# Kernel tuning notes

Hardware: AMD Instinct MI355X
Metric: run time of the kernel (lower is better)

## Reference

```python
import jax, jax.numpy as jnp
import numpy as np

Q_HEADS, KV_HEADS, D_K, D_V = 16, 4, 128, 128
GROUPS = Q_HEADS // KV_HEADS


def setup_inputs() -> dict:
    key = jax.random.key(0)
    ks = jax.random.split(key, 7)
    b, s, d = 2, 2048, 2048
    scale = 1.0 / np.sqrt(d).astype(np.float32)
    return {
        "Q": jax.random.normal(ks[0], (b, s, d), jnp.float32),
        "K": jax.random.normal(ks[1], (b, s, d), jnp.float32),
        "V": jax.random.normal(ks[2], (b, s, d), jnp.float32),
        "Wq": jax.random.normal(ks[3], (d, D_K * Q_HEADS), jnp.float32) * scale,
        "Wk": jax.random.normal(ks[4], (d, D_K * KV_HEADS), jnp.float32) * scale,
        "Wv": jax.random.normal(ks[5], (d, D_V * KV_HEADS), jnp.float32) * scale,
        "Wo": jax.random.normal(ks[6], (D_V * KV_HEADS, d), jnp.float32) * scale,
    }


def reference(Q, K, V, Wq, Wk, Wv, Wo):
    b, lq, _ = Q.shape
    lk = K.shape[1]
    # projections -> (b, heads, len, d)
    q = (Q @ Wq).reshape(b, lq, Q_HEADS, D_K).transpose(0, 2, 1, 3)
    k = (K @ Wk).reshape(b, lk, KV_HEADS, D_K).transpose(0, 2, 1, 3)
    v = (V @ Wv).reshape(b, lk, KV_HEADS, D_V).transpose(0, 2, 1, 3)
    # GQA quirk: scores summed over group dim g before softmax
    qr = q.reshape(b, GROUPS, KV_HEADS, lq, D_K)
    scores = jnp.einsum('bghqd,bhkd->bhqk', qr, k) / jnp.asarray(D_K ** 0.5, q.dtype)
    causal = jnp.tril(jnp.ones((lq, lk), bool))
    scores = jnp.where(causal[None, None], scores, jnp.asarray(-1e9, scores.dtype))
    attn = jax.nn.softmax(scores, axis=-1)  # (b, kv_heads, lq, lk)
    out = jnp.einsum('bhqk,bhkd->bhqd', attn, v)  # (b, kv_heads, lq, d_v)
    out = out.transpose(0, 2, 1, 3).reshape(b, lq, KV_HEADS * D_V)
    return out @ Wo
```

## Files before the change

### kernel.cpp

```cpp
#include <hip/hip_runtime.h>
#include <hip/hip_bf16.h>

typedef __attribute__((ext_vector_type(8))) short short8;
typedef __attribute__((ext_vector_type(4))) float f32x4;

#define MFMA16 __builtin_amdgcn_mfma_f32_16x16x32_bf16

__device__ inline unsigned short f2bf(float f) {
  __hip_bfloat16 h = __float2bfloat16(f);
  unsigned short u;
  __builtin_memcpy(&u, &h, 2);
  return u;
}

__device__ inline float bf2f(unsigned short u) {
  unsigned int x = ((unsigned int)u) << 16;
  float f;
  __builtin_memcpy(&f, &x, 4);
  return f;
}

__device__ inline void storeC(unsigned short* p, float v) { *p = f2bf(v); }
__device__ inline void storeC(float* p, float v) { *p = v; }

__device__ inline void gload16(const void* g, void* l) {
  __builtin_amdgcn_global_load_lds(
      (const __attribute__((address_space(1))) unsigned int*)g,
      (__attribute__((address_space(3))) unsigned int*)l,
      16, 0, 0);
}

__global__ __launch_bounds__(256)
void wqsum_t(const float* __restrict__ wq, unsigned short* __restrict__ dst) {
  __shared__ float t[64][65];
  const int n0 = blockIdx.x * 64, d0 = blockIdx.y * 64;
  const int tid = threadIdx.x;
#pragma unroll
  for (int it = 0; it < 16; ++it) {
    const int idx = it * 256 + tid;
    const int dd = idx >> 6, nn = idx & 63;
    const float* p = wq + (size_t)(d0 + dd) * 2048 + n0 + nn;
    t[dd][nn] = p[0] + p[512] + p[1024] + p[1536];
  }
  __syncthreads();
#pragma unroll
  for (int it = 0; it < 16; ++it) {
    const int idx = it * 256 + tid;
    const int nn = idx >> 6, dd = idx & 63;
    dst[(size_t)(n0 + nn) * 2048 + d0 + dd] = f2bf(t[dd][nn]);
  }
}

__global__ __launch_bounds__(256)
void transpose_w(const float* __restrict__ src, unsigned short* __restrict__ dst,
                 int R, int C) {
  __shared__ float t[64][65];
  const int c0 = blockIdx.x * 64, r0 = blockIdx.y * 64;
  const int tid = threadIdx.x;
#pragma unroll
  for (int it = 0; it < 16; ++it) {
    const int idx = it * 256 + tid;
    const int r = idx >> 6, c = idx & 63;
    t[r][c] = src[(size_t)(r0 + r) * C + c0 + c];
  }
  __syncthreads();
#pragma unroll
  for (int it = 0; it < 16; ++it) {
    const int idx = it * 256 + tid;
    const int rr = idx >> 6, cc = idx & 63;
    dst[(size_t)(c0 + rr) * R + r0 + cc] = f2bf(t[cc][rr]);
  }
}

__global__ __launch_bounds__(256)
void vtrans(const unsigned short* __restrict__ pC, unsigned short* __restrict__ vt) {
  __shared__ unsigned short t[64][72];
  const int s0 = blockIdx.x * 64;
  const int d0 = blockIdx.y * 64;
  const int bh = blockIdx.z;
  const int brow = (bh >> 2) * 2048;
  const int h = bh & 3;
  const int tid = threadIdx.x;
  const unsigned short* va = pC + 4194304;
  const unsigned short* vb = pC + 6291456 + 4194304;
#pragma unroll
  for (int it = 0; it < 2; ++it) {
    const int idx = it * 256 + tid;
    const int s = idx >> 3;
    const int dd = (idx & 7) << 3;
    const size_t off = (size_t)(brow + s0 + s) * 512 + h * 128 + d0 + dd;
    const short8 xa = *(const short8*)(va + off);
    const short8 xb = *(const short8*)(vb + off);
    short8 o;
#pragma unroll
    for (int e = 0; e < 8; ++e)
      o[e] = (short)f2bf(bf2f((unsigned short)xa[e]) + bf2f((unsigned short)xb[e]));
    *(short8*)&t[s][dd] = o;
  }
  __syncthreads();
#pragma unroll
  for (int it = 0; it < 2; ++it) {
    const int idx = it * 256 + tid;
    const int dd = idx >> 3;
    const int ss = (idx & 7) << 3;
    short8 o;
#pragma unroll
    for (int e = 0; e < 8; ++e) o[e] = (short)t[ss + e][dd];
    *(short8*)(vt + ((size_t)bh * 128 + d0 + dd) * 2048 + s0 + ss) = o;
  }
}

template <bool AF32, typename CT, int KS>
__global__ __launch_bounds__(256)
void gemm_bt(const void* A0, const void* A1, const void* A2,
             const unsigned short* __restrict__ Bt, CT* __restrict__ C,
             int K, int N, size_t sB, size_t sC) {
  __shared__ unsigned short As[AF32 ? 1 : 2][128 * 64];
  __shared__ unsigned short Bs[2][128 * 64];

  const int tid = threadIdx.x;
  const int lane = tid & 63;
  const int wv = tid >> 6;
  const int wm = (wv >> 1) << 6;
  const int wn = (wv & 1) << 6;
  const int l15 = lane & 15;
  const int l4 = lane >> 4;
  const int lsw = (l15 & 7) << 4;

  const int nwg = gridDim.x;
  const int bid = blockIdx.x;
  const int job = (bid & 7) * (nwg >> 3) + (bid >> 3);
  const int ntile = N >> 7;
  const int per_ks = nwg / KS;
  const int ks = (KS > 1) ? (job / per_ks) : 0;
  const int jj = job - ks * per_ks;
  const int z = jj / (32 * ntile);
  const int rem = jj - z * 32 * ntile;
  const int m0 = (rem / ntile) << 7;
  const int n0 = (rem % ntile) << 7;
  const int kbeg = ks * (K / KS);
  const int kend = kbeg + K / KS;

  const void* Az = (z == 0) ? A0 : (z == 1) ? A1 : A2;
  const unsigned short* Ab = (const unsigned short*)Az;
  const float* Af = (const float*)Az;
  const unsigned short* Bz = Bt + sB * (size_t)z;

  const f32x4 zero = {0.f, 0.f, 0.f, 0.f};
  f32x4 acc[4][4];
#pragma unroll
  for (int i = 0; i < 4; ++i)
#pragma unroll
    for (int j = 0; j < 4; ++j) acc[i][j] = zero;

  const int srow = tid >> 3;
  const int scol = (tid & 7) << 3;
  const int scolsw = scol ^ ((srow & 7) << 3);

  float4 ar[8];

  auto issueB = [&](int buf, int k0) {
#pragma unroll
    for (int s = 0; s < 4; ++s) {
      const unsigned short* bsrc =
          Bz + (size_t)(n0 + srow + s * 32) * K + k0 + scolsw;
      gload16(bsrc, (char*)&Bs[buf][0] + tid * 16 + s * 4096);
    }
  };
  auto issueA16 = [&](int buf, int k0) {
#pragma unroll
    for (int s = 0; s < 4; ++s) {
      const unsigned short* asrc =
          Ab + (size_t)(m0 + srow + s * 32) * K + k0 + scolsw;
      gload16(asrc, (char*)&As[buf][0] + tid * 16 + s * 4096);
    }
  };
  auto loadA = [&](int k0) {
#pragma unroll
    for (int s = 0; s < 4; ++s) {
      const float* asrc = Af + (size_t)(m0 + srow + s * 32) * K + k0 + scol;
      ar[2 * s] = *(const float4*)(asrc);
      ar[2 * s + 1] = *(const float4*)(asrc + 4);
    }
  };
  auto writeA = [&]() {
#pragma unroll
    for (int s = 0; s < 4; ++s) {
      short8 o;
      o[0] = (short)f2bf(ar[2 * s].x); o[1] = (short)f2bf(ar[2 * s].y);
      o[2] = (short)f2bf(ar[2 * s].z); o[3] = (short)f2bf(ar[2 * s].w);
      o[4] = (short)f2bf(ar[2 * s + 1].x); o[5] = (short)f2bf(ar[2 * s + 1].y);
      o[6] = (short)f2bf(ar[2 * s + 1].z); o[7] = (short)f2bf(ar[2 * s + 1].w);
      *(short8*)((char*)&As[0][0] + (srow + s * 32) * 128 + scolsw * 2) = o;
    }
  };

  if constexpr (AF32) loadA(kbeg); else issueA16(0, kbeg);
  issueB(0, kbeg);

  int cur = 0;
  for (int k0 = kbeg; k0 < kend; k0 += 64) {
    const bool more = (k0 + 64 < kend);
    asm volatile("s_waitcnt vmcnt(0)" ::: "memory");
    if constexpr (AF32) {
      writeA();
      if (more) { issueB(cur ^ 1, k0 + 64); loadA(k0 + 64); }
      asm volatile("s_waitcnt lgkmcnt(0)" ::: "memory");
    } else {
      if (more) { issueA16(cur ^ 1, k0 + 64); issueB(cur ^ 1, k0 + 64); }
    }
    __builtin_amdgcn_s_barrier();
    const unsigned short* as = AF32 ? &As[0][0] : &As[cur][0];
#pragma unroll
    for (int kk = 0; kk < 2; ++kk) {
      const int kb = (kk * 64 + (l4 << 4)) ^ lsw;
      short8 a[4], b[4];
#pragma unroll
      for (int i = 0; i < 4; ++i)
        a[i] = *(const short8*)((const char*)as + (wm + i * 16 + l15) * 128 + kb);
#pragma unroll
      for (int j = 0; j < 4; ++j)
        b[j] = *(const short8*)((const char*)&Bs[cur][0] +
                                (wn + j * 16 + l15) * 128 + kb);
#pragma unroll
      for (int i = 0; i < 4; ++i)
#pragma unroll
        for (int j = 0; j < 4; ++j)
          acc[i][j] = MFMA16(a[i], b[j], acc[i][j], 0, 0, 0);
    }
    __builtin_amdgcn_s_barrier();
    cur ^= 1;
  }

  CT* Cz = C + sC * (size_t)(ks * 3 + z);
#pragma unroll
  for (int i = 0; i < 4; ++i) {
    const int row0 = m0 + wm + i * 16 + (l4 << 2);
#pragma unroll
    for (int j = 0; j < 4; ++j) {
      const int col = n0 + wn + j * 16 + l15;
#pragma unroll
      for (int r = 0; r < 4; ++r)
        storeC(&Cz[(size_t)(row0 + r) * N + col], acc[i][j][r]);
    }
  }
}

__global__ __launch_bounds__(256)
void qkv_combine(const unsigned short* __restrict__ pC,
                 unsigned short* __restrict__ dst) {
  const size_t COUNT = 4194304;
  const size_t OFF = 6291456;
  size_t i = ((size_t)blockIdx.x * 256 + threadIdx.x) * 8;
  const size_t stride = (size_t)gridDim.x * 256 * 8;
  for (; i < COUNT; i += stride) {
    const short8 a = *(const short8*)(pC + i);
    const short8 b = *(const short8*)(pC + OFF + i);
    short8 o;
#pragma unroll
    for (int e = 0; e < 8; ++e)
      o[e] = (short)f2bf(bf2f((unsigned short)a[e]) + bf2f((unsigned short)b[e]));
    *(short8*)(dst + i) = o;
  }
}

__global__ __launch_bounds__(128, 1)
void attn_split(const unsigned short* __restrict__ qh,
                const unsigned short* __restrict__ kh,
                const unsigned short* __restrict__ vt,
                unsigned short* __restrict__ Oh,
                unsigned short* __restrict__ pO,
                float* __restrict__ pml) {
  __shared__ unsigned short P_lds[2][32][36];
  const int tid = threadIdx.x;
  const int lane = tid & 63;
  const int wave = tid >> 6;
  const int l15 = lane & 15;
  const int l4 = lane >> 4;
  const int bh = blockIdx.x & 7;
  const int jid = 143 - (int)(blockIdx.x >> 3);
  const int brow = (bh >> 2) * 2048;
  const int h = bh & 3;

  int j = jid, g = 0;
  while (j >= 2 * (g + 1) * (g + 2)) ++g;
  const int rem = j - 2 * g * (g + 1);
  const int r_ = rem / (g + 1);
  const int c_ = rem - r_ * (g + 1);
  const int qt = 4 * g + r_;
  const int k_begin = c_ << 8;
  const int k_end = (c_ == g) ? (qt + 1) * 64 : ((c_ + 1) << 8);
  const int qrow_w = qt * 64 + wave * 32;
  const float SCALE2 = 0.127517424f;

  short8 qf[2][4];
#pragma unroll
  for (int m = 0; m < 2; ++m) {
    const unsigned short* qp =
        qh + (size_t)(brow + qrow_w + m * 16 + l15) * 512 + h * 128 + (l4 << 3);
#pragma unroll
    for (int kk = 0; kk < 4; ++kk) qf[m][kk] = *(const short8*)(qp + kk * 32);
  }

  short8 oneb;
#pragma unroll
  for (int e = 0; e < 8; ++e) oneb[e] = (short)0x3F80;

  const f32x4 zero = {0.f, 0.f, 0.f, 0.f};
  f32x4 o_acc[2][8];
  f32x4 l_acc[2];
#pragma unroll
  for (int m = 0; m < 2; ++m) {
    l_acc[m] = zero;
#pragma unroll
    for (int i = 0; i < 8; ++i) o_acc[m][i] = zero;
  }

  const int nt = (k_end - k_begin) >> 5;
  for (int t = 0; t < nt; ++t) {
    const int kbase = k_begin + t * 32;
    if (kbase > qrow_w + 31) continue;
    short8 vb[8];
#pragma unroll
    for (int d8 = 0; d8 < 8; ++d8)
      vb[d8] = *(const short8*)(
          vt + ((size_t)bh * 128 + d8 * 16 + l15) * 2048 + kbase + (l4 << 3));
    short8 kf[2][4];
#pragma unroll
    for (int n = 0; n < 2; ++n) {
      const unsigned short* kp =
          kh + (size_t)(brow + kbase + n * 16 + l15) * 512 + h * 128 + (l4 << 3);
#pragma unroll
      for (int kk = 0; kk < 4; ++kk) kf[n][kk] = *(const short8*)(kp + kk * 32);
    }
    f32x4 sa[2][2];
    sa[0][0] = zero; sa[0][1] = zero; sa[1][0] = zero; sa[1][1] = zero;
#pragma unroll
    for (int n = 0; n < 2; ++n)
#pragma unroll
      for (int kk = 0; kk < 4; ++kk) {
        sa[0][n] = MFMA16(qf[0][kk], kf[n][kk], sa[0][n], 0, 0, 0);
        sa[1][n] = MFMA16(qf[1][kk], kf[n][kk], sa[1][n], 0, 0, 0);
      }
    const bool need_mask = (kbase + 31 > qrow_w);
    float p[2][2][4];
#pragma unroll
    for (int m = 0; m < 2; ++m)
#pragma unroll
      for (int n = 0; n < 2; ++n)
#pragma unroll
        for (int r = 0; r < 4; ++r) {
          const float v = exp2f(sa[m][n][r] * SCALE2 - 24.f);
          bool msk = false;
          if (need_mask) {
            const int kc = kbase + n * 16 + l15;
            const int qr = qrow_w + m * 16 + (l4 << 2) + r;
            msk = (kc > qr);
          }
          p[m][n][r] = msk ? 0.f : v;
        }
#pragma unroll
    for (int m = 0; m < 2; ++m)
#pragma unroll
      for (int n = 0; n < 2; ++n)
#pragma unroll
        for (int r = 0; r < 4; ++r)
          P_lds[wave][m * 16 + (l4 << 2) + r][n * 16 + l15] = f2bf(p[m][n][r]);
    short8 pa[2];
#pragma unroll
    for (int m = 0; m < 2; ++m)
      pa[m] = *(const short8*)((const char*)&P_lds[wave][0][0] +
                               (m * 16 + l15) * 72 + (l4 << 4));
    l_acc[0] = MFMA16(pa[0], oneb, l_acc[0], 0, 0, 0);
    l_acc[1] = MFMA16(pa[1], oneb, l_acc[1], 0, 0, 0);
#pragma unroll
    for (int d8 = 0; d8 < 8; ++d8) {
      o_acc[0][d8] = MFMA16(pa[0], vb[d8], o_acc[0][d8], 0, 0, 0);
      o_acc[1][d8] = MFMA16(pa[1], vb[d8], o_acc[1][d8], 0, 0, 0);
    }
  }

  if (g == 0) {
#pragma unroll
    for (int m = 0; m < 2; ++m)
#pragma unroll
      for (int d8 = 0; d8 < 8; ++d8)
#pragma unroll
        for (int r = 0; r < 4; ++r) {
          const int row = brow + qrow_w + m * 16 + (l4 << 2) + r;
          Oh[(size_t)row * 512 + h * 128 + d8 * 16 + l15] =
              f2bf(o_acc[m][d8][r] / l_acc[m][r]);
        }
  } else {
    const int slot = bh * 144 + jid;
    unsigned short* po = pO + (size_t)slot * 64 * 128;
#pragma unroll
    for (int m = 0; m < 2; ++m)
#pragma unroll
      for (int d8 = 0; d8 < 8; ++d8)
#pragma unroll
        for (int r = 0; r < 4; ++r) {
          const int row = wave * 32 + m * 16 + (l4 << 2) + r;
          po[row * 128 + d8 * 16 + l15] = f2bf(o_acc[m][d8][r]);
        }
    if (l15 == 0) {
#pragma unroll
      for (int m = 0; m < 2; ++m)
#pragma unroll
        for (int r = 0; r < 4; ++r) {
          const int row = wave * 32 + m * 16 + (l4 << 2) + r;
          pml[((size_t)slot * 64 + row) * 2 + 0] = 0.f;
          pml[((size_t)slot * 64 + row) * 2 + 1] = l_acc[m][r];
        }
    }
  }
}

__global__ __launch_bounds__(256)
void attn_combine(const unsigned short* __restrict__ pO,
                  const float* __restrict__ pml,
                  unsigned short* __restrict__ Oh) {
  const int bh = blockIdx.y;
  const int qt = 4 + blockIdx.x;
  const int g = qt >> 2;
  const int nch = g + 1;
  const int base = 2 * g * (g + 1) + (qt & 3) * (g + 1);
  const int slot0 = bh * 144 + base;
  const int brow = (bh >> 2) * 2048;
  const int h = bh & 3;
#pragma unroll
  for (int u = 0; u < 4; ++u) {
    const int unit = u * 256 + threadIdx.x;
    const int row = unit >> 4;
    const int c8 = (unit & 15) << 3;
    float M = -1e30f;
    for (int c = 0; c < nch; ++c)
      M = fmaxf(M, pml[((size_t)(slot0 + c) * 64 + row) * 2]);
    float L = 0.f;
    float acc[8] = {0.f, 0.f, 0.f, 0.f, 0.f, 0.f, 0.f, 0.f};
    for (int c = 0; c < nch; ++c) {
      const float mc = pml[((size_t)(slot0 + c) * 64 + row) * 2];
      const float lc = pml[((size_t)(slot0 + c) * 64 + row) * 2 + 1];
      const float w = exp2f(mc - M);
      L += w * lc;
      const short8 ov =
          *(const short8*)(pO + ((size_t)(slot0 + c) * 64 + row) * 128 + c8);
#pragma unroll
      for (int e = 0; e < 8; ++e) acc[e] += w * bf2f((unsigned short)ov[e]);
    }
    const float inv = 1.f / L;
    short8 o;
#pragma unroll
    for (int e = 0; e < 8; ++e) o[e] = (short)f2bf(acc[e] * inv);
    *(short8*)(Oh + (size_t)(brow + qt * 64 + row) * 512 + h * 128 + c8) = o;
  }
}

extern "C" void kernel_launch(void* const* d_in, const int* in_sizes, int n_in,
                              void* d_out, int out_size, void* d_ws, size_t ws_size,
                              hipStream_t stream) {
  const float* Q  = (const float*)d_in[0];
  const float* K_ = (const float*)d_in[1];
  const float* V  = (const float*)d_in[2];
  const float* Wq = (const float*)d_in[3];
  const float* Wk = (const float*)d_in[4];
  const float* Wv = (const float*)d_in[5];
  const float* Wo = (const float*)d_in[6];
  float* out = (float*)d_out;

  char* ws = (char*)d_ws;
  unsigned short* Wt  = (unsigned short*)ws;
  unsigned short* WoT = (unsigned short*)(ws + 6291456);
  unsigned short* qh  = (unsigned short*)(ws + 8388608);
  unsigned short* kh  = qh + 2097152;
  unsigned short* Oh  = qh + 3 * 2097152;
  unsigned short* vt  = (unsigned short*)(ws + 25165824);
  unsigned short* pO  = (unsigned short*)(ws + 29360128);
  float*          pml = (float*)(ws + 48234496);
  unsigned short* pC  = (unsigned short*)(ws + 20971520);

  wqsum_t<<<dim3(8, 32), 256, 0, stream>>>(Wq, Wt);
  transpose_w<<<dim3(8, 32), 256, 0, stream>>>(Wk, Wt + 1048576, 2048, 512);
  transpose_w<<<dim3(8, 32), 256, 0, stream>>>(Wv, Wt + 2097152, 2048, 512);
  transpose_w<<<dim3(32, 8), 256, 0, stream>>>(Wo, WoT, 512, 2048);

  gemm_bt<true, unsigned short, 2><<<768, 256, 0, stream>>>(
      Q, K_, V, Wt, pC, 2048, 512, 1048576, 2097152);
  qkv_combine<<<1024, 256, 0, stream>>>(pC, qh);
  vtrans<<<dim3(32, 2, 8), 256, 0, stream>>>(pC, vt);

  attn_split<<<1152, 128, 0, stream>>>(qh, kh, vt, Oh, pO, pml);
  attn_combine<<<dim3(28, 8), 256, 0, stream>>>(pO, pml, Oh);

  gemm_bt<false, float, 1><<<512, 256, 0, stream>>>(
      Oh, Oh, Oh, WoT, out, 512, 2048, 0, 0);
}
```

Baseline: 146.7 us.

## Double-buffer fp32 A tiles in LDS and prefetch two tiles ahead

In the fp32-input GEMM path, the A tile now gets two LDS buffers and two register staging sets, so global loads of A run two k-tiles ahead. The bf16 conversion and LDS write for the next tile happen after the MFMA work on the current tile. Partial vmcnt waits replace full drains. This is meant to hide global load latency that the single-buffer scheme left exposed, at the cost of more LDS and registers, which can lower occupancy.

```diff
diff --git a/kernel.cpp b/kernel.cpp
--- a/kernel.cpp
+++ b/kernel.cpp
@@ -115,7 +115,7 @@
 void gemm_bt(const void* A0, const void* A1, const void* A2,
              const unsigned short* __restrict__ Bt, CT* __restrict__ C,
              int K, int N, size_t sB, size_t sC) {
-  __shared__ unsigned short As[AF32 ? 1 : 2][128 * 64];
+  __shared__ unsigned short As[2][128 * 64];
   __shared__ unsigned short Bs[2][128 * 64];
 
   const int tid = threadIdx.x;
@@ -157,8 +157,6 @@
   const int scol = (tid & 7) << 3;
   const int scolsw = scol ^ ((srow & 7) << 3);
 
-  float4 ar[8];
-
   auto issueB = [&](int buf, int k0) {
 #pragma unroll
     for (int s = 0; s < 4; ++s) {
@@ -175,7 +173,7 @@
       gload16(asrc, (char*)&As[buf][0] + tid * 16 + s * 4096);
     }
   };
-  auto loadA = [&](int k0) {
+  auto loadAr = [&](float4 (&ar)[8], int k0) {
 #pragma unroll
     for (int s = 0; s < 4; ++s) {
       const float* asrc = Af + (size_t)(m0 + srow + s * 32) * K + k0 + scol;
@@ -183,7 +181,7 @@
       ar[2 * s + 1] = *(const float4*)(asrc + 4);
     }
   };
-  auto writeA = [&]() {
+  auto writeAr = [&](int buf, float4 (&ar)[8]) {
 #pragma unroll
     for (int s = 0; s < 4; ++s) {
       short8 o;
@@ -191,33 +189,18 @@
       o[2] = (short)f2bf(ar[2 * s].z); o[3] = (short)f2bf(ar[2 * s].w);
       o[4] = (short)f2bf(ar[2 * s + 1].x); o[5] = (short)f2bf(ar[2 * s + 1].y);
       o[6] = (short)f2bf(ar[2 * s + 1].z); o[7] = (short)f2bf(ar[2 * s + 1].w);
-      *(short8*)((char*)&As[0][0] + (srow + s * 32) * 128 + scolsw * 2) = o;
+      *(short8*)((char*)&As[buf][0] + (srow + s * 32) * 128 + scolsw * 2) = o;
     }
   };
-
-  if constexpr (AF32) loadA(kbeg); else issueA16(0, kbeg);
-  issueB(0, kbeg);
-
-  int cur = 0;
-  for (int k0 = kbeg; k0 < kend; k0 += 64) {
-    const bool more = (k0 + 64 < kend);
-    asm volatile("s_waitcnt vmcnt(0)" ::: "memory");
-    if constexpr (AF32) {
-      writeA();
-      if (more) { issueB(cur ^ 1, k0 + 64); loadA(k0 + 64); }
-      asm volatile("s_waitcnt lgkmcnt(0)" ::: "memory");
-    } else {
-      if (more) { issueA16(cur ^ 1, k0 + 64); issueB(cur ^ 1, k0 + 64); }
-    }
-    __builtin_amdgcn_s_barrier();
-    const unsigned short* as = AF32 ? &As[0][0] : &As[cur][0];
+  auto mfma_tile = [&](int cur) {
 #pragma unroll
     for (int kk = 0; kk < 2; ++kk) {
       const int kb = (kk * 64 + (l4 << 4)) ^ lsw;
       short8 a[4], b[4];
 #pragma unroll
       for (int i = 0; i < 4; ++i)
-        a[i] = *(const short8*)((const char*)as + (wm + i * 16 + l15) * 128 + kb);
+        a[i] = *(const short8*)((const char*)&As[cur][0] +
+                                (wm + i * 16 + l15) * 128 + kb);
 #pragma unroll
       for (int j = 0; j < 4; ++j)
         b[j] = *(const short8*)((const char*)&Bs[cur][0] +
@@ -228,8 +211,55 @@
         for (int j = 0; j < 4; ++j)
           acc[i][j] = MFMA16(a[i], b[j], acc[i][j], 0, 0, 0);
     }
-    __builtin_amdgcn_s_barrier();
-    cur ^= 1;
+  };
+
+  const int ntiles = (kend - kbeg) >> 6;
+
+  if constexpr (AF32) {
+    float4 arA[8], arB[8];
+    loadAr(arA, kbeg);
+    issueB(0, kbeg);
+    if (ntiles > 1) {
+      loadAr(arB, kbeg + 64);
+      asm volatile("s_waitcnt vmcnt(8)" ::: "memory");
+    } else {
+      asm volatile("s_waitcnt vmcnt(0)" ::: "memory");
+    }
+    writeAr(0, arA);
+
+    auto step = [&](int i, int cur, float4 (&arW)[8], float4 (&arL)[8]) {
+      if (i >= ntiles) return;
+      const bool haveB = (i + 1 < ntiles);
+      const bool haveA = (i + 2 < ntiles);
+      if (haveB) issueB(cur ^ 1, kbeg + (i + 1) * 64);
+      if (haveA) loadAr(arL, kbeg + (i + 2) * 64);
+      asm volatile("s_waitcnt lgkmcnt(0)" ::: "memory");
+      __builtin_amdgcn_s_barrier();
+      mfma_tile(cur);
+      if (haveB) {
+        if (haveA) asm volatile("s_waitcnt vmcnt(8)" ::: "memory");
+        else       asm volatile("s_waitcnt vmcnt(0)" ::: "memory");
+        __builtin_amdgcn_s_barrier();
+        writeAr(cur ^ 1, arW);
+      }
+    };
+    for (int i = 0; i < ntiles; i += 2) {
+      step(i, 0, arB, arA);
+      step(i + 1, 1, arA, arB);
+    }
+  } else {
+    issueA16(0, kbeg);
+    issueB(0, kbeg);
+    int cur = 0;
+    for (int k0 = kbeg; k0 < kend; k0 += 64) {
+      const bool more = (k0 + 64 < kend);
+      asm volatile("s_waitcnt vmcnt(0)" ::: "memory");
+      if (more) { issueA16(cur ^ 1, k0 + 64); issueB(cur ^ 1, k0 + 64); }
+      __builtin_amdgcn_s_barrier();
+      mfma_tile(cur);
+      __builtin_amdgcn_s_barrier();
+      cur ^= 1;
+    }
   }
 
   CT* Cz = C + sC * (size_t)(ks * 3 + z);
```

Measured after the change: 154.8 us. 1.06x slower.

## Use 3-way split-K for QKV GEMM and 4-wave 16-row attention blocks

Applied to the files above, without the earlier changes.

The QKV projection GEMM moves from a 2-way to a 3-way K split, launching more workgroups, and a third partial slot is summed in qkv_combine and vtrans. The f32-A path drops B double-buffering to cut LDS use. The attention split kernel now uses 4 waves of 16 query rows each instead of 2 waves of 32, which lowers per-wave register pressure so launch bounds can allow multiple blocks per CU. The workspace layout is reshuffled so the larger partial buffer overlaps regions that are already consumed. The costs are extra partial-sum traffic and less pipelining in the GEMM's B loads.

```diff
diff --git a/kernel.cpp b/kernel.cpp
--- a/kernel.cpp
+++ b/kernel.cpp
@@ -81,20 +81,24 @@
   const int brow = (bh >> 2) * 2048;
   const int h = bh & 3;
   const int tid = threadIdx.x;
-  const unsigned short* va = pC + 4194304;
-  const unsigned short* vb = pC + 6291456 + 4194304;
+  const unsigned short* v0 = pC + 4194304;
+  const unsigned short* v1 = pC + 6291456 + 4194304;
+  const unsigned short* v2 = pC + 12582912 + 4194304;
 #pragma unroll
   for (int it = 0; it < 2; ++it) {
     const int idx = it * 256 + tid;
     const int s = idx >> 3;
     const int dd = (idx & 7) << 3;
     const size_t off = (size_t)(brow + s0 + s) * 512 + h * 128 + d0 + dd;
-    const short8 xa = *(const short8*)(va + off);
-    const short8 xb = *(const short8*)(vb + off);
+    const short8 xa = *(const short8*)(v0 + off);
+    const short8 xb = *(const short8*)(v1 + off);
+    const short8 xc = *(const short8*)(v2 + off);
     short8 o;
 #pragma unroll
     for (int e = 0; e < 8; ++e)
-      o[e] = (short)f2bf(bf2f((unsigned short)xa[e]) + bf2f((unsigned short)xb[e]));
+      o[e] = (short)f2bf(bf2f((unsigned short)xa[e]) +
+                         bf2f((unsigned short)xb[e]) +
+                         bf2f((unsigned short)xc[e]));
     *(short8*)&t[s][dd] = o;
   }
   __syncthreads();
@@ -116,7 +120,7 @@
              const unsigned short* __restrict__ Bt, CT* __restrict__ C,
              int K, int N, size_t sB, size_t sC) {
   __shared__ unsigned short As[AF32 ? 1 : 2][128 * 64];
-  __shared__ unsigned short Bs[2][128 * 64];
+  __shared__ unsigned short Bs[AF32 ? 1 : 2][128 * 64];
 
   const int tid = threadIdx.x;
   const int lane = tid & 63;
@@ -138,8 +142,10 @@
   const int rem = jj - z * 32 * ntile;
   const int m0 = (rem / ntile) << 7;
   const int n0 = (rem % ntile) << 7;
-  const int kbeg = ks * (K / KS);
-  const int kend = kbeg + K / KS;
+  const int steps = K >> 6;
+  const int per = (steps + KS - 1) / KS;
+  const int sb = ks * per, se = (ks + 1) * per < steps ? (ks + 1) * per : steps;
+  const int kbeg = sb << 6, kend = se << 6;
 
   const void* Az = (z == 0) ? A0 : (z == 1) ? A1 : A2;
   const unsigned short* Ab = (const unsigned short*)Az;
@@ -194,30 +200,15 @@
       *(short8*)((char*)&As[0][0] + (srow + s * 32) * 128 + scolsw * 2) = o;
     }
   };
-
-  if constexpr (AF32) loadA(kbeg); else issueA16(0, kbeg);
-  issueB(0, kbeg);
-
-  int cur = 0;
-  for (int k0 = kbeg; k0 < kend; k0 += 64) {
-    const bool more = (k0 + 64 < kend);
-    asm volatile("s_waitcnt vmcnt(0)" ::: "memory");
-    if constexpr (AF32) {
-      writeA();
-      if (more) { issueB(cur ^ 1, k0 + 64); loadA(k0 + 64); }
-      asm volatile("s_waitcnt lgkmcnt(0)" ::: "memory");
-    } else {
-      if (more) { issueA16(cur ^ 1, k0 + 64); issueB(cur ^ 1, k0 + 64); }
-    }
-    __builtin_amdgcn_s_barrier();
-    const unsigned short* as = AF32 ? &As[0][0] : &As[cur][0];
+  auto mfma_tile = [&](int cur) {
 #pragma unroll
     for (int kk = 0; kk < 2; ++kk) {
       const int kb = (kk * 64 + (l4 << 4)) ^ lsw;
       short8 a[4], b[4];
 #pragma unroll
       for (int i = 0; i < 4; ++i)
-        a[i] = *(const short8*)((const char*)as + (wm + i * 16 + l15) * 128 + kb);
+        a[i] = *(const short8*)((const char*)&As[cur][0] +
+                                (wm + i * 16 + l15) * 128 + kb);
 #pragma unroll
       for (int j = 0; j < 4; ++j)
         b[j] = *(const short8*)((const char*)&Bs[cur][0] +
@@ -228,8 +219,31 @@
         for (int j = 0; j < 4; ++j)
           acc[i][j] = MFMA16(a[i], b[j], acc[i][j], 0, 0, 0);
     }
-    __builtin_amdgcn_s_barrier();
-    cur ^= 1;
+  };
+
+  if constexpr (AF32) {
+    loadA(kbeg);
+    for (int k0 = kbeg; k0 < kend; k0 += 64) {
+      writeA();
+      issueB(0, k0);
+      if (k0 + 64 < kend) loadA(k0 + 64);
+      __syncthreads();
+      mfma_tile(0);
+      __syncthreads();
+    }
+  } else {
+    issueA16(0, kbeg);
+    issueB(0, kbeg);
+    int cur = 0;
+    for (int k0 = kbeg; k0 < kend; k0 += 64) {
+      const bool more = (k0 + 64 < kend);
+      asm volatile("s_waitcnt vmcnt(0)" ::: "memory");
+      if (more) { issueA16(cur ^ 1, k0 + 64); issueB(cur ^ 1, k0 + 64); }
+      __builtin_amdgcn_s_barrier();
+      mfma_tile(cur);
+      __builtin_amdgcn_s_barrier();
+      cur ^= 1;
+    }
   }
 
   CT* Cz = C + sC * (size_t)(ks * 3 + z);
@@ -250,28 +264,31 @@
 void qkv_combine(const unsigned short* __restrict__ pC,
                  unsigned short* __restrict__ dst) {
   const size_t COUNT = 4194304;
-  const size_t OFF = 6291456;
+  const size_t SLOT = 6291456;
   size_t i = ((size_t)blockIdx.x * 256 + threadIdx.x) * 8;
   const size_t stride = (size_t)gridDim.x * 256 * 8;
   for (; i < COUNT; i += stride) {
     const short8 a = *(const short8*)(pC + i);
-    const short8 b = *(const short8*)(pC + OFF + i);
+    const short8 b = *(const short8*)(pC + SLOT + i);
+    const short8 c = *(const short8*)(pC + 2 * SLOT + i);
     short8 o;
 #pragma unroll
     for (int e = 0; e < 8; ++e)
-      o[e] = (short)f2bf(bf2f((unsigned short)a[e]) + bf2f((unsigned short)b[e]));
+      o[e] = (short)f2bf(bf2f((unsigned short)a[e]) +
+                         bf2f((unsigned short)b[e]) +
+                         bf2f((unsigned short)c[e]));
     *(short8*)(dst + i) = o;
   }
 }
 
-__global__ __launch_bounds__(128, 1)
+__global__ __launch_bounds__(256, 3)
 void attn_split(const unsigned short* __restrict__ qh,
                 const unsigned short* __restrict__ kh,
                 const unsigned short* __restrict__ vt,
                 unsigned short* __restrict__ Oh,
                 unsigned short* __restrict__ pO,
                 float* __restrict__ pml) {
-  __shared__ unsigned short P_lds[2][32][36];
+  __shared__ unsigned short P_lds[4][16][36];
   const int tid = threadIdx.x;
   const int lane = tid & 63;
   const int wave = tid >> 6;
@@ -290,16 +307,15 @@
   const int qt = 4 * g + r_;
   const int k_begin = c_ << 8;
   const int k_end = (c_ == g) ? (qt + 1) * 64 : ((c_ + 1) << 8);
-  const int qrow_w = qt * 64 + wave * 32;
+  const int qrow_w = qt * 64 + wave * 16;
   const float SCALE2 = 0.127517424f;
 
-  short8 qf[2][4];
-#pragma unroll
-  for (int m = 0; m < 2; ++m) {
+  short8 qf[4];
+  {
     const unsigned short* qp =
-        qh + (size_t)(brow + qrow_w + m * 16 + l15) * 512 + h * 128 + (l4 << 3);
-#pragma unroll
-    for (int kk = 0; kk < 4; ++kk) qf[m][kk] = *(const short8*)(qp + kk * 32);
+        qh + (size_t)(brow + qrow_w + l15) * 512 + h * 128 + (l4 << 3);
+#pragma unroll
+    for (int kk = 0; kk < 4; ++kk) qf[kk] = *(const short8*)(qp + kk * 32);
   }
 
   short8 oneb;
@@ -307,111 +323,95 @@
   for (int e = 0; e < 8; ++e) oneb[e] = (short)0x3F80;
 
   const f32x4 zero = {0.f, 0.f, 0.f, 0.f};
-  f32x4 o_acc[2][8];
-  f32x4 l_acc[2];
-#pragma unroll
-  for (int m = 0; m < 2; ++m) {
-    l_acc[m] = zero;
-#pragma unroll
-    for (int i = 0; i < 8; ++i) o_acc[m][i] = zero;
-  }
+  f32x4 o_acc[8];
+  f32x4 l_acc = zero;
+#pragma unroll
+  for (int i = 0; i < 8; ++i) o_acc[i] = zero;
 
   const int nt = (k_end - k_begin) >> 5;
   for (int t = 0; t < nt; ++t) {
     const int kbase = k_begin + t * 32;
-    if (kbase > qrow_w + 31) continue;
-    short8 vb[8];
-#pragma unroll
-    for (int d8 = 0; d8 < 8; ++d8)
-      vb[d8] = *(const short8*)(
+    if (kbase > qrow_w + 15) continue;
+    short8 vb0[4];
+#pragma unroll
+    for (int d8 = 0; d8 < 4; ++d8)
+      vb0[d8] = *(const short8*)(
           vt + ((size_t)bh * 128 + d8 * 16 + l15) * 2048 + kbase + (l4 << 3));
-    short8 kf[2][4];
+    f32x4 sa[2];
+    sa[0] = zero; sa[1] = zero;
 #pragma unroll
     for (int n = 0; n < 2; ++n) {
+      short8 kf[4];
       const unsigned short* kp =
           kh + (size_t)(brow + kbase + n * 16 + l15) * 512 + h * 128 + (l4 << 3);
 #pragma unroll
-      for (int kk = 0; kk < 4; ++kk) kf[n][kk] = *(const short8*)(kp + kk * 32);
-    }
-    f32x4 sa[2][2];
-    sa[0][0] = zero; sa[0][1] = zero; sa[1][0] = zero; sa[1][1] = zero;
+      for (int kk = 0; kk < 4; ++kk) kf[kk] = *(const short8*)(kp + kk * 32);
+#pragma unroll
+      for (int kk = 0; kk < 4; ++kk)
+        sa[n] = MFMA16(qf[kk], kf[kk], sa[n], 0, 0, 0);
+    }
+    const bool need_mask = (kbase + 31 > qrow_w);
+    float p[2][4];
 #pragma unroll
     for (int n = 0; n < 2; ++n)
 #pragma unroll
-      for (int kk = 0; kk < 4; ++kk) {
-        sa[0][n] = MFMA16(qf[0][kk], kf[n][kk], sa[0][n], 0, 0, 0);
-        sa[1][n] = MFMA16(qf[1][kk], kf[n][kk], sa[1][n], 0, 0, 0);
+      for (int r = 0; r < 4; ++r) {
+        const float v = exp2f(sa[n][r] * SCALE2 - 24.f);
+        bool msk = false;
+        if (need_mask) {
+          const int kc = kbase + n * 16 + l15;
+          const int qr = qrow_w + (l4 << 2) + r;
+          msk = (kc > qr);
+        }
+        p[n][r] = msk ? 0.f : v;
       }
-    const bool need_mask = (kbase + 31 > qrow_w);
-    float p[2][2][4];
-#pragma unroll
-    for (int m = 0; m < 2; ++m)
-#pragma unroll
-      for (int n = 0; n < 2; ++n)
-#pragma unroll
-        for (int r = 0; r < 4; ++r) {
-          const float v = exp2f(sa[m][n][r] * SCALE2 - 24.f);
-          bool msk = false;
-          if (need_mask) {
-            const int kc = kbase + n * 16 + l15;
-            const int qr = qrow_w + m * 16 + (l4 << 2) + r;
-            msk = (kc > qr);
-          }
-          p[m][n][r] = msk ? 0.f : v;
-        }
-#pragma unroll
-    for (int m = 0; m < 2; ++m)
-#pragma unroll
-      for (int n = 0; n < 2; ++n)
-#pragma unroll
-        for (int r = 0; r < 4; ++r)
-          P_lds[wave][m * 16 + (l4 << 2) + r][n * 16 + l15] = f2bf(p[m][n][r]);
-    short8 pa[2];
-#pragma unroll
-    for (int m = 0; m < 2; ++m)
-      pa[m] = *(const short8*)((const char*)&P_lds[wave][0][0] +
-                               (m * 16 + l15) * 72 + (l4 << 4));
-    l_acc[0] = MFMA16(pa[0], oneb, l_acc[0], 0, 0, 0);
-    l_acc[1] = MFMA16(pa[1], oneb, l_acc[1], 0, 0, 0);
-#pragma unroll
-    for (int d8 = 0; d8 < 8; ++d8) {
-      o_acc[0][d8] = MFMA16(pa[0], vb[d8], o_acc[0][d8], 0, 0, 0);
-      o_acc[1][d8] = MFMA16(pa[1], vb[d8], o_acc[1][d8], 0, 0, 0);
-    }
+#pragma unroll
+    for (int n = 0; n < 2; ++n)
+#pragma unroll
+      for (int r = 0; r < 4; ++r)
+        P_lds[wave][(l4 << 2) + r][n * 16 + l15] = f2bf(p[n][r]);
+    short8 pa = *(const short8*)((const char*)&P_lds[wave][0][0] +
+                                 l15 * 72 + (l4 << 4));
+    short8 vb1[4];
+#pragma unroll
+    for (int d8 = 0; d8 < 4; ++d8)
+      vb1[d8] = *(const short8*)(
+          vt + ((size_t)bh * 128 + (d8 + 4) * 16 + l15) * 2048 + kbase + (l4 << 3));
+    l_acc = MFMA16(pa, oneb, l_acc, 0, 0, 0);
+#pragma unroll
+    for (int d8 = 0; d8 < 4; ++d8)
+      o_acc[d8] = MFMA16(pa, vb0[d8], o_acc[d8], 0, 0, 0);
+#pragma unroll
+    for (int d8 = 0; d8 < 4; ++d8)
+      o_acc[d8 + 4] = MFMA16(pa, vb1[d8], o_acc[d8 + 4], 0, 0, 0);
   }
 
   if (g == 0) {
 #pragma unroll
-    for (int m = 0; m < 2; ++m)
-#pragma unroll
-      for (int d8 = 0; d8 < 8; ++d8)
-#pragma unroll
-        for (int r = 0; r < 4; ++r) {
-          const int row = brow + qrow_w + m * 16 + (l4 << 2) + r;
-          Oh[(size_t)row * 512 + h * 128 + d8 * 16 + l15] =
-              f2bf(o_acc[m][d8][r] / l_acc[m][r]);
-        }
+    for (int d8 = 0; d8 < 8; ++d8)
+#pragma unroll
+      for (int r = 0; r < 4; ++r) {
+        const int row = brow + qrow_w + (l4 << 2) + r;
+        Oh[(size_t)row * 512 + h * 128 + d8 * 16 + l15] =
+            f2bf(o_acc[d8][r] / l_acc[r]);
+      }
   } else {
     const int slot = bh * 144 + jid;
     unsigned short* po = pO + (size_t)slot * 64 * 128;
 #pragma unroll
-    for (int m = 0; m < 2; ++m)
-#pragma unroll
-      for (int d8 = 0; d8 < 8; ++d8)
-#pragma unroll
-        for (int r = 0; r < 4; ++r) {
-          const int row = wave * 32 + m * 16 + (l4 << 2) + r;
-          po[row * 128 + d8 * 16 + l15] = f2bf(o_acc[m][d8][r]);
-        }
+    for (int d8 = 0; d8 < 8; ++d8)
+#pragma unroll
+      for (int r = 0; r < 4; ++r) {
+        const int row = wave * 16 + (l4 << 2) + r;
+        po[row * 128 + d8 * 16 + l15] = f2bf(o_acc[d8][r]);
+      }
     if (l15 == 0) {
 #pragma unroll
-      for (int m = 0; m < 2; ++m)
-#pragma unroll
-        for (int r = 0; r < 4; ++r) {
-          const int row = wave * 32 + m * 16 + (l4 << 2) + r;
-          pml[((size_t)slot * 64 + row) * 2 + 0] = 0.f;
-          pml[((size_t)slot * 64 + row) * 2 + 1] = l_acc[m][r];
-        }
+      for (int r = 0; r < 4; ++r) {
+        const int row = wave * 16 + (l4 << 2) + r;
+        pml[((size_t)slot * 64 + row) * 2 + 0] = 0.f;
+        pml[((size_t)slot * 64 + row) * 2 + 1] = l_acc[r];
+      }
     }
   }
 }
@@ -473,23 +473,23 @@
   unsigned short* WoT = (unsigned short*)(ws + 6291456);
   unsigned short* qh  = (unsigned short*)(ws + 8388608);
   unsigned short* kh  = qh + 2097152;
-  unsigned short* Oh  = qh + 3 * 2097152;
+  unsigned short* Oh  = (unsigned short*)(ws + 20971520);
   unsigned short* vt  = (unsigned short*)(ws + 25165824);
   unsigned short* pO  = (unsigned short*)(ws + 29360128);
   float*          pml = (float*)(ws + 48234496);
-  unsigned short* pC  = (unsigned short*)(ws + 20971520);
+  unsigned short* pC  = (unsigned short*)(ws + 8388608);
 
   wqsum_t<<<dim3(8, 32), 256, 0, stream>>>(Wq, Wt);
   transpose_w<<<dim3(8, 32), 256, 0, stream>>>(Wk, Wt + 1048576, 2048, 512);
   transpose_w<<<dim3(8, 32), 256, 0, stream>>>(Wv, Wt + 2097152, 2048, 512);
   transpose_w<<<dim3(32, 8), 256, 0, stream>>>(Wo, WoT, 512, 2048);
 
-  gemm_bt<true, unsigned short, 2><<<768, 256, 0, stream>>>(
+  gemm_bt<true, unsigned short, 3><<<1152, 256, 0, stream>>>(
       Q, K_, V, Wt, pC, 2048, 512, 1048576, 2097152);
   qkv_combine<<<1024, 256, 0, stream>>>(pC, qh);
   vtrans<<<dim3(32, 2, 8), 256, 0, stream>>>(pC, vt);
 
-  attn_split<<<1152, 128, 0, stream>>>(qh, kh, vt, Oh, pO, pml);
+  attn_split<<<1152, 256, 0, stream>>>(qh, kh, vt, Oh, pO, pml);
   attn_combine<<<dim3(28, 8), 256, 0, stream>>>(pO, pml, Oh);
 
   gemm_bt<false, float, 1><<<512, 256, 0, stream>>>(
```

Measured after the change: 190.1 us. +29.6%, slower.

## Pack Q/K/V into MFMA fragment order and double-buffer attention loads

Applied to the files above, without the earlier changes.

Replaces the row-major combine kernel and the V transpose with packing kernels that write Q, K and V directly in per-lane MFMA fragment order. Each lane's short8 is then contiguous, so attention loads are fully coalesced instead of strided row gathers. The attention inner loop also gains two-stage register double-buffering of K/V tiles, and fully masked tiles are dropped from the loop bound instead of being skipped with a branch. The cost is more registers under a 128-thread, 1-block launch bound, plus tighter workspace aliasing, since vpack reuses the partial-sum buffer.

```diff
diff --git a/kernel.cpp b/kernel.cpp
--- a/kernel.cpp
+++ b/kernel.cpp
@@ -69,44 +69,6 @@
     const int idx = it * 256 + tid;
     const int rr = idx >> 6, cc = idx & 63;
     dst[(size_t)(c0 + rr) * R + r0 + cc] = f2bf(t[cc][rr]);
-  }
-}
-
-__global__ __launch_bounds__(256)
-void vtrans(const unsigned short* __restrict__ pC, unsigned short* __restrict__ vt) {
-  __shared__ unsigned short t[64][72];
-  const int s0 = blockIdx.x * 64;
-  const int d0 = blockIdx.y * 64;
-  const int bh = blockIdx.z;
-  const int brow = (bh >> 2) * 2048;
-  const int h = bh & 3;
-  const int tid = threadIdx.x;
-  const unsigned short* va = pC + 4194304;
-  const unsigned short* vb = pC + 6291456 + 4194304;
-#pragma unroll
-  for (int it = 0; it < 2; ++it) {
-    const int idx = it * 256 + tid;
-    const int s = idx >> 3;
-    const int dd = (idx & 7) << 3;
-    const size_t off = (size_t)(brow + s0 + s) * 512 + h * 128 + d0 + dd;
-    const short8 xa = *(const short8*)(va + off);
-    const short8 xb = *(const short8*)(vb + off);
-    short8 o;
-#pragma unroll
-    for (int e = 0; e < 8; ++e)
-      o[e] = (short)f2bf(bf2f((unsigned short)xa[e]) + bf2f((unsigned short)xb[e]));
-    *(short8*)&t[s][dd] = o;
-  }
-  __syncthreads();
-#pragma unroll
-  for (int it = 0; it < 2; ++it) {
-    const int idx = it * 256 + tid;
-    const int dd = idx >> 3;
-    const int ss = (idx & 7) << 3;
-    short8 o;
-#pragma unroll
-    for (int e = 0; e < 8; ++e) o[e] = (short)t[ss + e][dd];
-    *(short8*)(vt + ((size_t)bh * 128 + d0 + dd) * 2048 + s0 + ss) = o;
   }
 }
 
@@ -247,27 +209,82 @@
 }
 
 __global__ __launch_bounds__(256)
-void qkv_combine(const unsigned short* __restrict__ pC,
-                 unsigned short* __restrict__ dst) {
-  const size_t COUNT = 4194304;
-  const size_t OFF = 6291456;
-  size_t i = ((size_t)blockIdx.x * 256 + threadIdx.x) * 8;
-  const size_t stride = (size_t)gridDim.x * 256 * 8;
-  for (; i < COUNT; i += stride) {
-    const short8 a = *(const short8*)(pC + i);
-    const short8 b = *(const short8*)(pC + OFF + i);
+void qkv_pack(const unsigned short* __restrict__ pC,
+              unsigned short* __restrict__ qpack,
+              unsigned short* __restrict__ kpack) {
+  const size_t SLOTE = 6291456;
+  const int idx = blockIdx.x * 256 + threadIdx.x;
+  const int lane = idx & 63;
+  const int kk = (idx >> 6) & 3;
+  const int qb = (idx >> 8) & 127;
+  const int bh = idx >> 15;
+  const int row = (bh >> 2) * 2048 + qb * 16 + (lane & 15);
+  const int col = (bh & 3) * 128 + kk * 32 + (lane >> 4) * 8;
+  const size_t off = (size_t)row * 512 + col;
+  {
+    const short8 a = *(const short8*)(pC + off);
+    const short8 b = *(const short8*)(pC + SLOTE + off);
     short8 o;
 #pragma unroll
     for (int e = 0; e < 8; ++e)
       o[e] = (short)f2bf(bf2f((unsigned short)a[e]) + bf2f((unsigned short)b[e]));
-    *(short8*)(dst + i) = o;
+    *(short8*)(qpack + (size_t)idx * 8) = o;
+  }
+  {
+    const short8 a = *(const short8*)(pC + 2097152 + off);
+    const short8 b = *(const short8*)(pC + SLOTE + 2097152 + off);
+    short8 o;
+#pragma unroll
+    for (int e = 0; e < 8; ++e)
+      o[e] = (short)f2bf(bf2f((unsigned short)a[e]) + bf2f((unsigned short)b[e]));
+    *(short8*)(kpack + (size_t)idx * 8) = o;
+  }
+}
+
+__global__ __launch_bounds__(256)
+void vpack_k(const unsigned short* __restrict__ pC,
+             unsigned short* __restrict__ vpack) {
+  __shared__ unsigned short t[32][132];
+  const int kvb = blockIdx.x;
+  const int bh = blockIdx.y;
+  const int brow = (bh >> 2) * 2048;
+  const int h = bh & 3;
+  const int tid = threadIdx.x;
+  const unsigned short* v0 = pC + 4194304;
+  const unsigned short* v1 = pC + 6291456 + 4194304;
+#pragma unroll
+  for (int it = 0; it < 2; ++it) {
+    const int idx = it * 256 + tid;
+    const int r = idx >> 4;
+    const int c8 = (idx & 15) << 3;
+    const size_t off = (size_t)(brow + kvb * 32 + r) * 512 + h * 128 + c8;
+    const short8 xa = *(const short8*)(v0 + off);
+    const short8 xb = *(const short8*)(v1 + off);
+    short8 o;
+#pragma unroll
+    for (int e = 0; e < 8; ++e)
+      o[e] = (short)f2bf(bf2f((unsigned short)xa[e]) + bf2f((unsigned short)xb[e]));
+    *(short8*)&t[r][c8] = o;
+  }
+  __syncthreads();
+#pragma unroll
+  for (int it = 0; it < 2; ++it) {
+    const int idx = it * 256 + tid;
+    const int d8 = idx >> 6;
+    const int lane = idx & 63;
+    const int l15 = lane & 15;
+    const int l4 = lane >> 4;
+    short8 o;
+#pragma unroll
+    for (int e = 0; e < 8; ++e) o[e] = (short)t[l4 * 8 + e][d8 * 16 + l15];
+    *(short8*)(vpack + ((((size_t)bh * 64 + kvb) * 8 + d8) * 64 + lane) * 8) = o;
   }
 }
 
 __global__ __launch_bounds__(128, 1)
-void attn_split(const unsigned short* __restrict__ qh,
-                const unsigned short* __restrict__ kh,
-                const unsigned short* __restrict__ vt,
+void attn_split(const unsigned short* __restrict__ qpack,
+                const unsigned short* __restrict__ kpack,
+                const unsigned short* __restrict__ vpack,
                 unsigned short* __restrict__ Oh,
                 unsigned short* __restrict__ pO,
                 float* __restrict__ pml) {
@@ -295,12 +312,11 @@
 
   short8 qf[2][4];
 #pragma unroll
-  for (int m = 0; m < 2; ++m) {
-    const unsigned short* qp =
-        qh + (size_t)(brow + qrow_w + m * 16 + l15) * 512 + h * 128 + (l4 << 3);
-#pragma unroll
-    for (int kk = 0; kk < 4; ++kk) qf[m][kk] = *(const short8*)(qp + kk * 32);
-  }
+  for (int m = 0; m < 2; ++m)
+#pragma unroll
+    for (int kk = 0; kk < 4; ++kk)
+      qf[m][kk] = *(const short8*)(qpack +
+          ((((size_t)bh * 128 + (qrow_w >> 4) + m) * 4 + kk) * 64 + lane) * 8);
 
   short8 oneb;
 #pragma unroll
@@ -317,22 +333,27 @@
   }
 
   const int nt = (k_end - k_begin) >> 5;
-  for (int t = 0; t < nt; ++t) {
+  int ntv = ((qrow_w + 31 - k_begin) >> 5) + 1;
+  if (ntv > nt) ntv = nt;
+
+  auto loadK = [&](short8 (&kf)[2][4], int t) {
+    const int kvb = (k_begin >> 4) + t * 2;
+#pragma unroll
+    for (int n = 0; n < 2; ++n)
+#pragma unroll
+      for (int kk = 0; kk < 4; ++kk)
+        kf[n][kk] = *(const short8*)(kpack +
+            ((((size_t)bh * 128 + kvb + n) * 4 + kk) * 64 + lane) * 8);
+  };
+  auto loadV = [&](short8 (&vb)[8], int t) {
+    const int kvb32 = (k_begin >> 5) + t;
+#pragma unroll
+    for (int d8 = 0; d8 < 8; ++d8)
+      vb[d8] = *(const short8*)(vpack +
+          ((((size_t)bh * 64 + kvb32) * 8 + d8) * 64 + lane) * 8);
+  };
+  auto compute = [&](int t, short8 (&kf)[2][4], short8 (&vb)[8]) {
     const int kbase = k_begin + t * 32;
-    if (kbase > qrow_w + 31) continue;
-    short8 vb[8];
-#pragma unroll
-    for (int d8 = 0; d8 < 8; ++d8)
-      vb[d8] = *(const short8*)(
-          vt + ((size_t)bh * 128 + d8 * 16 + l15) * 2048 + kbase + (l4 << 3));
-    short8 kf[2][4];
-#pragma unroll
-    for (int n = 0; n < 2; ++n) {
-      const unsigned short* kp =
-          kh + (size_t)(brow + kbase + n * 16 + l15) * 512 + h * 128 + (l4 << 3);
-#pragma unroll
-      for (int kk = 0; kk < 4; ++kk) kf[n][kk] = *(const short8*)(kp + kk * 32);
-    }
     f32x4 sa[2][2];
     sa[0][0] = zero; sa[0][1] = zero; sa[1][0] = zero; sa[1][1] = zero;
 #pragma unroll
@@ -377,6 +398,18 @@
     for (int d8 = 0; d8 < 8; ++d8) {
       o_acc[0][d8] = MFMA16(pa[0], vb[d8], o_acc[0][d8], 0, 0, 0);
       o_acc[1][d8] = MFMA16(pa[1], vb[d8], o_acc[1][d8], 0, 0, 0);
+    }
+  };
+
+  short8 kfA[2][4], vbA[8], kfB[2][4], vbB[8];
+  loadK(kfA, 0);
+  loadV(vbA, 0);
+  for (int t = 0; t < ntv; t += 2) {
+    if (t + 1 < ntv) { loadK(kfB, t + 1); loadV(vbB, t + 1); }
+    compute(t, kfA, vbA);
+    if (t + 1 < ntv) {
+      if (t + 2 < ntv) { loadK(kfA, t + 2); loadV(vbA, t + 2); }
+      compute(t + 1, kfB, vbB);
     }
   }
 
@@ -469,15 +502,15 @@
   float* out = (float*)d_out;
 
   char* ws = (char*)d_ws;
-  unsigned short* Wt  = (unsigned short*)ws;
-  unsigned short* WoT = (unsigned short*)(ws + 6291456);
-  unsigned short* qh  = (unsigned short*)(ws + 8388608);
-  unsigned short* kh  = qh + 2097152;
-  unsigned short* Oh  = qh + 3 * 2097152;
-  unsigned short* vt  = (unsigned short*)(ws + 25165824);
-  unsigned short* pO  = (unsigned short*)(ws + 29360128);
-  float*          pml = (float*)(ws + 48234496);
-  unsigned short* pC  = (unsigned short*)(ws + 20971520);
+  unsigned short* Wt    = (unsigned short*)ws;
+  unsigned short* WoT   = (unsigned short*)(ws + 6291456);
+  unsigned short* qpack = (unsigned short*)(ws + 8388608);
+  unsigned short* kpack = (unsigned short*)(ws + 12582912);
+  unsigned short* Oh    = (unsigned short*)(ws + 16777216);
+  unsigned short* pC    = (unsigned short*)(ws + 20971520);
+  unsigned short* vpack = (unsigned short*)(ws + 20971520);
+  unsigned short* pO    = (unsigned short*)(ws + 25165824);
+  float*          pml   = (float*)(ws + 48234496);
 
   wqsum_t<<<dim3(8, 32), 256, 0, stream>>>(Wq, Wt);
   transpose_w<<<dim3(8, 32), 256, 0, stream>>>(Wk, Wt + 1048576, 2048, 512);
@@ -486,10 +519,10 @@
 
   gemm_bt<true, unsigned short, 2><<<768, 256, 0, stream>>>(
       Q, K_, V, Wt, pC, 2048, 512, 1048576, 2097152);
-  qkv_combine<<<1024, 256, 0, stream>>>(pC, qh);
-  vtrans<<<dim3(32, 2, 8), 256, 0, stream>>>(pC, vt);
-
-  attn_split<<<1152, 128, 0, stream>>>(qh, kh, vt, Oh, pO, pml);
+  qkv_pack<<<1024, 256, 0, stream>>>(pC, qpack, kpack);
+  vpack_k<<<dim3(64, 8), 256, 0, stream>>>(pC, vpack);
+
+  attn_split<<<1152, 128, 0, stream>>>(qpack, kpack, vpack, Oh, pO, pml);
   attn_combine<<<dim3(28, 8), 256, 0, stream>>>(pO, pml, Oh);
 
   gemm_bt<false, float, 1><<<512, 256, 0, stream>>>(
```

After: 134.8 us. -8.1%, faster.
